# Optimization experiments

Hardware: AMD Instinct MI355X
Metric: run time of the kernel (lower is better)

## Reference

```python
import jax, jax.numpy as jnp
import numpy as np

HIDDEN = 1024
B, S = 4, 2048


def setup_inputs() -> dict:
    key = jax.random.key(0)
    ks = jax.random.split(key, 8)
    scale = 1.0 / np.sqrt(HIDDEN)
    return {
        "hidden_states": jax.random.normal(ks[0], (B, S, HIDDEN), dtype=jnp.float32),
        "attention_mask": jnp.zeros((B, S, S), dtype=jnp.float32),
        "Wq": jax.random.normal(ks[1], (HIDDEN, HIDDEN), dtype=jnp.float32) * scale,
        "bq": jnp.zeros((HIDDEN,), dtype=jnp.float32),
        "Wk": jax.random.normal(ks[2], (HIDDEN, HIDDEN), dtype=jnp.float32) * scale,
        "bk": jnp.zeros((HIDDEN,), dtype=jnp.float32),
        "Wv": jax.random.normal(ks[3], (HIDDEN, HIDDEN), dtype=jnp.float32) * scale,
        "bv": jnp.zeros((HIDDEN,), dtype=jnp.float32),
    }


def reference(hidden_states, attention_mask, Wq, bq, Wk, bk, Wv, bv):
    # Dense projections (note: no head split in the original module)
    q = jnp.einsum('bsd,de->bse', hidden_states, Wq) + bq  # [B,S,H]
    k = jnp.einsum('bsd,de->bse', hidden_states, Wk) + bk
    v = jnp.einsum('bsd,de->bse', hidden_states, Wv) + bv
    # scores scaled by sqrt(hidden_size) (not per-head dim), per the source
    inv_scale = 1.0 / jnp.sqrt(jnp.asarray(q.shape[-1], dtype=q.dtype))
    scores = jnp.einsum('bqd,bkd->bqk', q, k) * inv_scale  # [B,S,S]
    scores = scores + attention_mask
    weights = jax.nn.softmax(scores, axis=-1)
    # dropout is identity (training=False)
    out = jnp.einsum('bqk,bkd->bqd', weights, v)  # [B,S,H]
    return out
```

## Files before the change

### kernel.cpp

```cpp
#include <hip/hip_runtime.h>
#include <stdint.h>

typedef __attribute__((ext_vector_type(8))) short short8;
typedef __attribute__((ext_vector_type(8))) unsigned short u16x8;
typedef __attribute__((ext_vector_type(4))) float f32x4;

__device__ __forceinline__ uint16_t f2bf(float x) {
  uint32_t u = __float_as_uint(x);
  uint32_t r = (u + 0x7FFFu + ((u >> 16) & 1u)) >> 16;
  return (uint16_t)r;
}
__device__ __forceinline__ float bf2f(uint16_t x) {
  return __uint_as_float(((uint32_t)x) << 16);
}

__device__ __forceinline__ void gl_lds16(const uint16_t* g, void* l) {
  __builtin_amdgcn_global_load_lds(
      (const __attribute__((address_space(1))) void*)g,
      (__attribute__((address_space(3))) void*)l, 16, 0, 0);
}


__global__ __launch_bounds__(256) void cvt_f32_to_bf16(const float* __restrict__ in,
                                                       uint16_t* __restrict__ out) {
  long i = ((long)blockIdx.x * 256 + threadIdx.x) * 8;
  f32x4 v0 = *(const f32x4*)(in + i);
  f32x4 v1 = *(const f32x4*)(in + i + 4);
  u16x8 o;
  o[0] = f2bf(v0[0]); o[1] = f2bf(v0[1]); o[2] = f2bf(v0[2]); o[3] = f2bf(v0[3]);
  o[4] = f2bf(v1[0]); o[5] = f2bf(v1[1]); o[6] = f2bf(v1[2]); o[7] = f2bf(v1[3]);
  *(u16x8*)(out + i) = o;
}

__global__ __launch_bounds__(64) void cvt_w_transpose(const float* __restrict__ W0,
                                                      const float* __restrict__ W1,
                                                      const float* __restrict__ W2,
                                                      uint16_t* __restrict__ WT) {
  const int z = blockIdx.z;
  const float* W = (z == 0) ? W0 : ((z == 1) ? W1 : W2);
  uint16_t* out = WT + (long)z * 1024 * 1024;
  const int n = blockIdx.x * 64 + threadIdx.x;
  const int k0 = blockIdx.y * 128;
  for (int kk = 0; kk < 128; kk += 8) {
    u16x8 o;
#pragma unroll
    for (int j = 0; j < 8; j++) o[j] = f2bf(W[(long)(k0 + kk + j) * 1024 + n]);
    *(u16x8*)(out + (long)n * 1024 + k0 + kk) = o;
  }
}

__global__ __launch_bounds__(256) void transpose_v(const uint16_t* __restrict__ V,
                                                   uint16_t* __restrict__ Vt) {
  __shared__ uint16_t tile[64][66];
  const int b = blockIdx.z;
  const int s0 = blockIdx.x * 64, d0 = blockIdx.y * 64;
  const int t = threadIdx.x;
  const int r = t >> 3, c = (t & 7) * 8;
  const uint16_t* Vb = V + (long)b * 2048 * 1024;
#pragma unroll
  for (int j = 0; j < 2; j++) {
    u16x8 v = *(const u16x8*)(Vb + (long)(s0 + r + 32 * j) * 1024 + d0 + c);
#pragma unroll
    for (int i = 0; i < 8; i++) tile[r + 32 * j][c + i] = v[i];
  }
  __syncthreads();
  uint16_t* Vtb = Vt + (long)b * 1024 * 2048;
#pragma unroll
  for (int j = 0; j < 2; j++) {
    const int d = r + 32 * j;
    u16x8 o;
#pragma unroll
    for (int i = 0; i < 8; i++) o[i] = tile[c + i][d];
    *(u16x8*)(Vtb + (long)(d0 + d) * 2048 + s0 + c) = o;
  }
}

template <int MODE>
__global__ __launch_bounds__(512, 2) void gemm3(
    const uint16_t* __restrict__ Abase, long sAz,
    const uint16_t* __restrict__ Bbase, long sBz,
    int K, int N,
    char* __restrict__ Cbase, long sCz,
    const float* __restrict__ e0, const float* __restrict__ e1,
    const float* __restrict__ e2,
    const float* __restrict__ lsum) {
  constexpr int ABYTES = 256 * 32 * 2;
  constexpr int BBYTES = 128 * 32 * 2;
  constexpr int BUFB = ABYTES + BBYTES;
  __shared__ __align__(16) char lds[2 * BUFB];
  const int t = threadIdx.x;
  const int lane = t & 63;
  const int w = t >> 6;
  const int bm = blockIdx.x, bn = blockIdx.y, bz = blockIdx.z;
  const uint16_t* A = (const uint16_t*)((const char*)Abase + (long)bz * sAz);
  const uint16_t* Bm = (const uint16_t*)((const char*)Bbase + (long)bz * sBz);

  const int sr = t >> 2;
  const int sc = (t & 3) * 8;
  const uint16_t* ga0 = A + (long)(bm * 256 + sr) * K + sc;
  const uint16_t* ga1 = A + (long)(bm * 256 + 128 + sr) * K + sc;
  const uint16_t* gb0 = Bm + (long)(bn * 128 + sr) * K + sc;

  f32x4 acc[4][4];
#pragma unroll
  for (int i = 0; i < 4; i++)
#pragma unroll
    for (int j = 0; j < 4; j++) acc[i][j] = (f32x4){0.f, 0.f, 0.f, 0.f};

  const int wm = w >> 1, wn = w & 1;
  const int fr = lane & 15, kg = lane >> 4;
  const int aoff = (wm * 64 + fr) * 32 + kg * 8;
  const int boff = (wn * 64 + fr) * 32 + kg * 8;

#define STG(off, ko) { gl_lds16(ga0 + (ko), lds + (off) + w * 1024); \
                       gl_lds16(ga1 + (ko), lds + (off) + 8192 + w * 1024); \
                       gl_lds16(gb0 + (ko), lds + (off) + ABYTES + w * 1024); }

  STG(0, 0);

  int cur = 0;
  for (int k0 = 0; k0 < K; k0 += 32) {
    __syncthreads();
    if (k0 + 32 < K) {
      STG((cur ^ 1) * BUFB, k0 + 32);
    }
    const uint16_t* Ab = (const uint16_t*)(lds + cur * BUFB);
    const uint16_t* Bb = (const uint16_t*)(lds + cur * BUFB + ABYTES);
    short8 a[4], b[4];
#pragma unroll
    for (int i = 0; i < 4; i++) a[i] = *(const short8*)(Ab + aoff + i * 16 * 32);
#pragma unroll
    for (int j = 0; j < 4; j++) b[j] = *(const short8*)(Bb + boff + j * 16 * 32);
#pragma unroll
    for (int i = 0; i < 4; i++)
#pragma unroll
      for (int j = 0; j < 4; j++)
        acc[i][j] = __builtin_amdgcn_mfma_f32_16x16x32_bf16(a[i], b[j], acc[i][j], 0, 0, 0);
    cur ^= 1;
  }
#undef STG

  const int row0 = bm * 256 + wm * 64 + (kg << 2);
  if (MODE == 0) {
    const int zz = bn >> 3;
    const float* bias = (zz == 0) ? e0 : ((zz == 1) ? e1 : e2);
    uint16_t* C = (uint16_t*)(Cbase + (long)zz * sCz);
    const int cb = (bn & 7) * 128 + wn * 64 + fr;
#pragma unroll
    for (int i = 0; i < 4; i++) {
#pragma unroll
      for (int j = 0; j < 4; j++) {
        const float bv_ = bias[cb + j * 16];
#pragma unroll
        for (int r = 0; r < 4; r++) {
          C[(long)(row0 + i * 16 + r) * 1024 + cb + j * 16] = f2bf(acc[i][j][r] + bv_);
        }
      }
    }
  } else {
    const int col0 = bn * 128 + wn * 64 + fr;
    float* C = (float*)(Cbase + (long)bz * sCz);
    const float* ls = lsum + (long)bz * 2048;
#pragma unroll
    for (int i = 0; i < 4; i++) {
      const int rr = row0 + i * 16;
      const float ri0 = 1.0f / ls[rr], ri1 = 1.0f / ls[rr + 1];
      const float ri2 = 1.0f / ls[rr + 2], ri3 = 1.0f / ls[rr + 3];
#pragma unroll
      for (int j = 0; j < 4; j++) {
        float* dst = C + (long)rr * N + col0 + j * 16;
        dst[0] = acc[i][j][0] * ri0;
        dst[(long)N] = acc[i][j][1] * ri1;
        dst[(long)2 * N] = acc[i][j][2] * ri2;
        dst[(long)3 * N] = acc[i][j][3] * ri3;
      }
    }
  }
}

__global__ __launch_bounds__(512, 2) void gemm_sc(
    const uint16_t* __restrict__ Abase, long sAz,
    const uint16_t* __restrict__ Bbase, long sBz,
    int K, int N,
    char* __restrict__ Cbase, long sCz,
    const float* __restrict__ maskb, long sMz, float scale,
    float* __restrict__ lsum) {
  constexpr int ABYTES = 32768;
  constexpr int BUFB = 65536;
  __shared__ __align__(16) char lds[2 * BUFB];
  const int t = threadIdx.x;
  const int lane = t & 63;
  const int w = t >> 6;
  const int bm = blockIdx.x, bn = blockIdx.y, bz = blockIdx.z;
  const uint16_t* A = (const uint16_t*)((const char*)Abase + (long)bz * sAz);
  const uint16_t* B = (const uint16_t*)((const char*)Bbase + (long)bz * sBz);

  const int srow = t >> 3;
  const int scol = ((((t & 7) * 16) ^ ((srow & 7) << 4)) >> 1);
  const uint16_t* gA[4];
  const uint16_t* gB[4];
#pragma unroll
  for (int s = 0; s < 4; s++) {
    gA[s] = A + (long)(bm * 256 + s * 64 + srow) * K + scol;
    gB[s] = B + (long)(bn * 256 + s * 64 + srow) * K + scol;
  }

  const int wm = w >> 2, wn = w & 3;
  const int fr = lane & 15, kg = lane >> 4;
  const int X = (fr & 7) << 4;
  const int aRow = (wm * 128 + fr) * 128 + kg * 16;
  const int bRow = (wn * 64 + fr) * 128 + kg * 16;

  f32x4 acc[8][4];
#pragma unroll
  for (int i = 0; i < 8; i++)
#pragma unroll
    for (int j = 0; j < 4; j++) acc[i][j] = (f32x4){0.f, 0.f, 0.f, 0.f};

  short8 aR[4][2], bR[4][2];
  const int NT = K >> 6;

#define ARD(off, i, ks) (*(const short8*)(lds + (off) + ((aRow + (i) * 2048 + (ks) * 64) ^ X)))
#define BRD(off, j, ks) (*(const short8*)(lds + ABYTES + (off) + ((bRow + (j) * 2048 + (ks) * 64) ^ X)))
#define STG_A01(off, ko) { gl_lds16(gA[0] + (ko), lds + (off) + w * 1024); \
                           gl_lds16(gA[1] + (ko), lds + (off) + 8192 + w * 1024); }
#define STG_A23(off, ko) { gl_lds16(gA[2] + (ko), lds + (off) + 16384 + w * 1024); \
                           gl_lds16(gA[3] + (ko), lds + (off) + 24576 + w * 1024); }
#define STG_B01(off, ko) { gl_lds16(gB[0] + (ko), lds + ABYTES + (off) + w * 1024); \
                           gl_lds16(gB[1] + (ko), lds + ABYTES + (off) + 8192 + w * 1024); }
#define STG_B23(off, ko) { gl_lds16(gB[2] + (ko), lds + ABYTES + (off) + 16384 + w * 1024); \
                           gl_lds16(gB[3] + (ko), lds + ABYTES + (off) + 24576 + w * 1024); }
#define LGKM0 { asm volatile("s_waitcnt lgkmcnt(0)" ::: "memory"); __builtin_amdgcn_sched_barrier(0); }
#define MFMA16(I0, J0)                                                            \
  __builtin_amdgcn_s_setprio(1);                                                  \
  _Pragma("unroll") for (int i = 0; i < 4; i++)                                   \
  _Pragma("unroll") for (int j = 0; j < 2; j++)                                   \
  _Pragma("unroll") for (int ks = 0; ks < 2; ks++)                                \
    acc[(I0) + i][(J0) + j] = __builtin_amdgcn_mfma_f32_16x16x32_bf16(            \
        aR[i][ks], bR[(J0) + j][ks], acc[(I0) + i][(J0) + j], 0, 0, 0);           \
  __builtin_amdgcn_s_setprio(0);

  STG_A01(0, 0); STG_A23(0, 0); STG_B01(0, 0); STG_B23(0, 0);

  int curo = 0;
  for (int tt = 0; tt < NT - 1; ++tt) {
    const int nxto = curo ^ BUFB;
    const int ko = (tt + 1) << 6;
    STG_A01(nxto, ko);
    asm volatile("s_waitcnt vmcnt(2)" ::: "memory");
    __builtin_amdgcn_s_barrier();
    __builtin_amdgcn_sched_barrier(0);
#pragma unroll
    for (int i = 0; i < 4; i++) { aR[i][0] = ARD(curo, i, 0); aR[i][1] = ARD(curo, i, 1); }
#pragma unroll
    for (int j = 0; j < 4; j++) { bR[j][0] = BRD(curo, j, 0); bR[j][1] = BRD(curo, j, 1); }
    LGKM0;
    MFMA16(0, 0);
    __builtin_amdgcn_s_barrier();
    STG_A23(nxto, ko);
    __builtin_amdgcn_s_barrier();
    MFMA16(0, 2);
    __builtin_amdgcn_s_barrier();
    STG_B01(nxto, ko);
#pragma unroll
    for (int i = 0; i < 4; i++) { aR[i][0] = ARD(curo, 4 + i, 0); aR[i][1] = ARD(curo, 4 + i, 1); }
    __builtin_amdgcn_s_barrier();
    LGKM0;
    MFMA16(4, 2);
    __builtin_amdgcn_s_barrier();
    STG_B23(nxto, ko);
    __builtin_amdgcn_s_barrier();
    MFMA16(4, 0);
    __builtin_amdgcn_s_barrier();
    curo = nxto;
  }
  asm volatile("s_waitcnt vmcnt(0)" ::: "memory");
  __builtin_amdgcn_s_barrier();
  __builtin_amdgcn_sched_barrier(0);
#pragma unroll
  for (int i = 0; i < 4; i++) { aR[i][0] = ARD(curo, i, 0); aR[i][1] = ARD(curo, i, 1); }
#pragma unroll
  for (int j = 0; j < 4; j++) { bR[j][0] = BRD(curo, j, 0); bR[j][1] = BRD(curo, j, 1); }
  LGKM0;
  MFMA16(0, 0);
  MFMA16(0, 2);
#pragma unroll
  for (int i = 0; i < 4; i++) { aR[i][0] = ARD(curo, 4 + i, 0); aR[i][1] = ARD(curo, 4 + i, 1); }
  LGKM0;
  MFMA16(4, 2);
  MFMA16(4, 0);

  __syncthreads();
  constexpr int RS = 260;
  float* eL = (float*)lds;
  const int wboff = wm * (16 * RS) + (kg * 4) * RS + wn * 64 + fr;
  const int lr = t >> 4, slab = lr >> 4, row16 = lr & 15, cj = t & 15;
  const float* rb = eL + slab * (16 * RS) + row16 * RS + cj * 16;
  const int grow_base = bm * 256 + slab * 128 + row16;
  const int colg = bn * 256 + cj * 16;
  uint16_t* Cw = (uint16_t*)(Cbase + (long)bz * sCz);
  const float* mk = (const float*)((const char*)maskb + (long)bz * sMz);

#pragma unroll
  for (int i = 0; i < 8; i++) {
#pragma unroll
    for (int j = 0; j < 4; j++)
#pragma unroll
      for (int r = 0; r < 4; r++)
        eL[wboff + r * RS + j * 16] = acc[i][j][r];
    __syncthreads();
    f32x4 v0 = *(const f32x4*)(rb);
    f32x4 v1 = *(const f32x4*)(rb + 4);
    f32x4 v2 = *(const f32x4*)(rb + 8);
    f32x4 v3 = *(const f32x4*)(rb + 12);
    const int grow = grow_base + i * 16;
    const float* mrow = mk + (long)grow * N + colg;
    f32x4 m0 = *(const f32x4*)(mrow);
    f32x4 m1 = *(const f32x4*)(mrow + 4);
    f32x4 m2 = *(const f32x4*)(mrow + 8);
    f32x4 m3 = *(const f32x4*)(mrow + 12);
    float e[16];
#pragma unroll
    for (int q = 0; q < 4; q++) {
      e[q] = __expf(v0[q] * scale + m0[q]);
      e[4 + q] = __expf(v1[q] * scale + m1[q]);
      e[8 + q] = __expf(v2[q] * scale + m2[q]);
      e[12 + q] = __expf(v3[q] * scale + m3[q]);
    }
    float ps = 0.f;
#pragma unroll
    for (int q = 0; q < 16; q++) ps += e[q];
    ps += __shfl_xor(ps, 1);
    ps += __shfl_xor(ps, 2);
    ps += __shfl_xor(ps, 4);
    ps += __shfl_xor(ps, 8);
    if ((lane & 15) == 0) atomicAdd(lsum + (long)bz * 2048 + grow, ps);
    u16x8 o0, o1;
#pragma unroll
    for (int q = 0; q < 8; q++) { o0[q] = f2bf(e[q]); o1[q] = f2bf(e[8 + q]); }
    uint16_t* dst = Cw + (long)grow * N + colg;
    *(u16x8*)dst = o0;
    *(u16x8*)(dst + 8) = o1;
    __syncthreads();
  }
#undef ARD
#undef BRD
#undef STG_A01
#undef STG_A23
#undef STG_B01
#undef STG_B23
#undef LGKM0
#undef MFMA16
}

extern "C" void kernel_launch(void* const* d_in, const int* in_sizes, int n_in,
                              void* d_out, int out_size, void* d_ws, size_t ws_size,
                              hipStream_t stream) {
  const float* hs = (const float*)d_in[0];
  const float* mask = (const float*)d_in[1];
  const float* Wq = (const float*)d_in[2];
  const float* bq = (const float*)d_in[3];
  const float* Wk = (const float*)d_in[4];
  const float* bk = (const float*)d_in[5];
  const float* Wv = (const float*)d_in[6];
  const float* bv = (const float*)d_in[7];
  float* out = (float*)d_out;

  char* ws = (char*)d_ws;
  uint16_t* hsb = (uint16_t*)ws;
  uint16_t* WT = (uint16_t*)(ws + (16L << 20));
  uint16_t* QKV = (uint16_t*)(ws + (22L << 20));
  uint16_t* Vt = (uint16_t*)(ws + (70L << 20));
  uint16_t* E = (uint16_t*)(ws + (86L << 20));
  float* lsum = (float*)(ws + (118L << 20));

  cvt_f32_to_bf16<<<4096, 256, 0, stream>>>(hs, hsb);
  cvt_w_transpose<<<dim3(16, 8, 3), 64, 0, stream>>>(Wq, Wk, Wv, WT);
  hipMemsetAsync((void*)lsum, 0, 4L * 2048 * sizeof(float), stream);
  gemm3<0><<<dim3(32, 24, 1), 512, 0, stream>>>(
      hsb, 0L, WT, 0L, 1024, 3072, (char*)QKV, 16L << 20,
      bq, bk, bv, nullptr);
  transpose_v<<<dim3(32, 16, 4), 256, 0, stream>>>(QKV + 2L * 8192 * 1024, Vt);
  gemm_sc<<<dim3(8, 8, 4), 512, 0, stream>>>(
      QKV, 4L << 20, QKV + 8192L * 1024, 4L << 20, 1024, 2048, (char*)E, 8L << 20,
      mask, 16L << 20, 0.03125f, lsum);
  gemm3<2><<<dim3(8, 8, 4), 512, 0, stream>>>(
      E, 8L << 20, Vt, 4L << 20, 2048, 1024, (char*)out, 8L << 20,
      nullptr, nullptr, nullptr, lsum);
}
```

Before: 196.4 us.

## Remap GEMM block indices for XCD locality and shrink PV tile to 128x128

Result: no change. 197.9 us (+0.7%).

```diff
diff --git a/kernel.cpp b/kernel.cpp
--- a/kernel.cpp
+++ b/kernel.cpp
@@ -75,15 +75,12 @@
   }
 }
 
-template <int MODE>
-__global__ __launch_bounds__(512, 2) void gemm3(
-    const uint16_t* __restrict__ Abase, long sAz,
-    const uint16_t* __restrict__ Bbase, long sBz,
-    int K, int N,
+__global__ __launch_bounds__(512, 2) void gemm3_proj(
+    const uint16_t* __restrict__ A, const uint16_t* __restrict__ Bm,
     char* __restrict__ Cbase, long sCz,
     const float* __restrict__ e0, const float* __restrict__ e1,
-    const float* __restrict__ e2,
-    const float* __restrict__ lsum) {
+    const float* __restrict__ e2) {
+  constexpr int K = 1024;
   constexpr int ABYTES = 256 * 32 * 2;
   constexpr int BBYTES = 128 * 32 * 2;
   constexpr int BUFB = ABYTES + BBYTES;
@@ -91,9 +88,10 @@
   const int t = threadIdx.x;
   const int lane = t & 63;
   const int w = t >> 6;
-  const int bm = blockIdx.x, bn = blockIdx.y, bz = blockIdx.z;
-  const uint16_t* A = (const uint16_t*)((const char*)Abase + (long)bz * sAz);
-  const uint16_t* Bm = (const uint16_t*)((const char*)Bbase + (long)bz * sBz);
+  const int hw = blockIdx.x;
+  const int x = hw & 7, c = hw >> 3;
+  const int bm = ((x >> 1) << 3) + (c & 7);
+  const int bn = (x & 1) * 12 + (c >> 3);
 
   const int sr = t >> 2;
   const int sc = (t & 3) * 8;
@@ -115,17 +113,100 @@
 #define STG(off, ko) { gl_lds16(ga0 + (ko), lds + (off) + w * 1024); \
                        gl_lds16(ga1 + (ko), lds + (off) + 8192 + w * 1024); \
                        gl_lds16(gb0 + (ko), lds + (off) + ABYTES + w * 1024); }
-
   STG(0, 0);
+  int cur = 0;
+  for (int k0 = 0; k0 < K; k0 += 32) {
+    __syncthreads();
+    if (k0 + 32 < K) STG((cur ^ 1) * BUFB, k0 + 32);
+    const uint16_t* Ab = (const uint16_t*)(lds + cur * BUFB);
+    const uint16_t* Bb = (const uint16_t*)(lds + cur * BUFB + ABYTES);
+    short8 a[4], b[4];
+#pragma unroll
+    for (int i = 0; i < 4; i++) a[i] = *(const short8*)(Ab + aoff + i * 16 * 32);
+#pragma unroll
+    for (int j = 0; j < 4; j++) b[j] = *(const short8*)(Bb + boff + j * 16 * 32);
+#pragma unroll
+    for (int i = 0; i < 4; i++)
+#pragma unroll
+      for (int j = 0; j < 4; j++)
+        acc[i][j] = __builtin_amdgcn_mfma_f32_16x16x32_bf16(a[i], b[j], acc[i][j], 0, 0, 0);
+    cur ^= 1;
+  }
+#undef STG
+
+  const int row0 = bm * 256 + wm * 64 + (kg << 2);
+  const int zz = bn >> 3;
+  const float* bias = (zz == 0) ? e0 : ((zz == 1) ? e1 : e2);
+  uint16_t* C = (uint16_t*)(Cbase + (long)zz * sCz);
+  const int cb = (bn & 7) * 128 + wn * 64 + fr;
+#pragma unroll
+  for (int i = 0; i < 4; i++) {
+#pragma unroll
+    for (int j = 0; j < 4; j++) {
+      const float bv_ = bias[cb + j * 16];
+#pragma unroll
+      for (int r = 0; r < 4; r++) {
+        C[(long)(row0 + i * 16 + r) * 1024 + cb + j * 16] = f2bf(acc[i][j][r] + bv_);
+      }
+    }
+  }
+}
+
+__global__ __launch_bounds__(256) void gemm_pv(
+    const uint16_t* __restrict__ Abase, long sAz,
+    const uint16_t* __restrict__ Bbase, long sBz,
+    int K, int N,
+    float* __restrict__ Cbase, long sCzf,
+    const float* __restrict__ lsum) {
+  __shared__ uint16_t Al[2][128 * 32];
+  __shared__ uint16_t Bl[2][128 * 32];
+  const int t = threadIdx.x;
+  const int lane = t & 63;
+  const int w = t >> 6;
+  const int hw = blockIdx.x;
+  const int x = hw & 7, c = hw >> 3;
+  const int bz = x & 3;
+  const int bm = ((x >> 2) << 3) + (c & 7);
+  const int bn = c >> 3;
+
+  const uint16_t* A = (const uint16_t*)((const char*)Abase + (long)bz * sAz);
+  const uint16_t* Bm = (const uint16_t*)((const char*)Bbase + (long)bz * sBz);
+
+  const int sr = t >> 2;
+  const int sc = (t & 3) * 8;
+  const uint16_t* ga0 = A + (long)(bm * 128 + sr) * K + sc;
+  const uint16_t* ga1 = A + (long)(bm * 128 + 64 + sr) * K + sc;
+  const uint16_t* gb0 = Bm + (long)(bn * 128 + sr) * K + sc;
+  const uint16_t* gb1 = Bm + (long)(bn * 128 + 64 + sr) * K + sc;
+
+  f32x4 acc[4][4];
+#pragma unroll
+  for (int i = 0; i < 4; i++)
+#pragma unroll
+    for (int j = 0; j < 4; j++) acc[i][j] = (f32x4){0.f, 0.f, 0.f, 0.f};
+
+  const int wm = w >> 1, wn = w & 1;
+  const int fr = lane & 15, kg = lane >> 4;
+  const int aoff = (wm * 64 + fr) * 32 + kg * 8;
+  const int boff = (wn * 64 + fr) * 32 + kg * 8;
+
+  gl_lds16(ga0, Al[0] + w * 512);
+  gl_lds16(ga1, Al[0] + 2048 + w * 512);
+  gl_lds16(gb0, Bl[0] + w * 512);
+  gl_lds16(gb1, Bl[0] + 2048 + w * 512);
 
   int cur = 0;
   for (int k0 = 0; k0 < K; k0 += 32) {
     __syncthreads();
     if (k0 + 32 < K) {
-      STG((cur ^ 1) * BUFB, k0 + 32);
+      const int nb = cur ^ 1, kn = k0 + 32;
+      gl_lds16(ga0 + kn, Al[nb] + w * 512);
+      gl_lds16(ga1 + kn, Al[nb] + 2048 + w * 512);
+      gl_lds16(gb0 + kn, Bl[nb] + w * 512);
+      gl_lds16(gb1 + kn, Bl[nb] + 2048 + w * 512);
     }
-    const uint16_t* Ab = (const uint16_t*)(lds + cur * BUFB);
-    const uint16_t* Bb = (const uint16_t*)(lds + cur * BUFB + ABYTES);
+    const uint16_t* Ab = Al[cur];
+    const uint16_t* Bb = Bl[cur];
     short8 a[4], b[4];
 #pragma unroll
     for (int i = 0; i < 4; i++) a[i] = *(const short8*)(Ab + aoff + i * 16 * 32);
@@ -138,42 +219,23 @@
         acc[i][j] = __builtin_amdgcn_mfma_f32_16x16x32_bf16(a[i], b[j], acc[i][j], 0, 0, 0);
     cur ^= 1;
   }
-#undef STG
-
-  const int row0 = bm * 256 + wm * 64 + (kg << 2);
-  if (MODE == 0) {
-    const int zz = bn >> 3;
-    const float* bias = (zz == 0) ? e0 : ((zz == 1) ? e1 : e2);
-    uint16_t* C = (uint16_t*)(Cbase + (long)zz * sCz);
-    const int cb = (bn & 7) * 128 + wn * 64 + fr;
-#pragma unroll
-    for (int i = 0; i < 4; i++) {
-#pragma unroll
-      for (int j = 0; j < 4; j++) {
-        const float bv_ = bias[cb + j * 16];
-#pragma unroll
-        for (int r = 0; r < 4; r++) {
-          C[(long)(row0 + i * 16 + r) * 1024 + cb + j * 16] = f2bf(acc[i][j][r] + bv_);
-        }
-      }
-    }
-  } else {
-    const int col0 = bn * 128 + wn * 64 + fr;
-    float* C = (float*)(Cbase + (long)bz * sCz);
-    const float* ls = lsum + (long)bz * 2048;
-#pragma unroll
-    for (int i = 0; i < 4; i++) {
-      const int rr = row0 + i * 16;
-      const float ri0 = 1.0f / ls[rr], ri1 = 1.0f / ls[rr + 1];
-      const float ri2 = 1.0f / ls[rr + 2], ri3 = 1.0f / ls[rr + 3];
-#pragma unroll
-      for (int j = 0; j < 4; j++) {
-        float* dst = C + (long)rr * N + col0 + j * 16;
-        dst[0] = acc[i][j][0] * ri0;
-        dst[(long)N] = acc[i][j][1] * ri1;
-        dst[(long)2 * N] = acc[i][j][2] * ri2;
-        dst[(long)3 * N] = acc[i][j][3] * ri3;
-      }
+
+  const int row0 = bm * 128 + wm * 64 + (kg << 2);
+  const int col0 = bn * 128 + wn * 64 + fr;
+  float* C = Cbase + (long)bz * sCzf;
+  const float* ls = lsum + (long)bz * 2048;
+#pragma unroll
+  for (int i = 0; i < 4; i++) {
+    const int rr = row0 + i * 16;
+    const float ri0 = 1.0f / ls[rr], ri1 = 1.0f / ls[rr + 1];
+    const float ri2 = 1.0f / ls[rr + 2], ri3 = 1.0f / ls[rr + 3];
+#pragma unroll
+    for (int j = 0; j < 4; j++) {
+      float* dst = C + (long)rr * N + col0 + j * 16;
+      dst[0] = acc[i][j][0] * ri0;
+      dst[(long)N] = acc[i][j][1] * ri1;
+      dst[(long)2 * N] = acc[i][j][2] * ri2;
+      dst[(long)3 * N] = acc[i][j][3] * ri3;
     }
   }
 }
@@ -191,7 +253,11 @@
   const int t = threadIdx.x;
   const int lane = t & 63;
   const int w = t >> 6;
-  const int bm = blockIdx.x, bn = blockIdx.y, bz = blockIdx.z;
+  const int hw = blockIdx.x;
+  const int x = hw & 7, c = hw >> 3;
+  const int bz = x & 3;
+  const int bm = c & 7;
+  const int bn = ((x >> 2) << 2) + (c >> 3);
   const uint16_t* A = (const uint16_t*)((const char*)Abase + (long)bz * sAz);
   const uint16_t* B = (const uint16_t*)((const char*)Bbase + (long)bz * sBz);
 
@@ -377,14 +443,12 @@
   cvt_f32_to_bf16<<<4096, 256, 0, stream>>>(hs, hsb);
   cvt_w_transpose<<<dim3(16, 8, 3), 64, 0, stream>>>(Wq, Wk, Wv, WT);
   hipMemsetAsync((void*)lsum, 0, 4L * 2048 * sizeof(float), stream);
-  gemm3<0><<<dim3(32, 24, 1), 512, 0, stream>>>(
-      hsb, 0L, WT, 0L, 1024, 3072, (char*)QKV, 16L << 20,
-      bq, bk, bv, nullptr);
+  gemm3_proj<<<768, 512, 0, stream>>>(
+      hsb, WT, (char*)QKV, 16L << 20, bq, bk, bv);
   transpose_v<<<dim3(32, 16, 4), 256, 0, stream>>>(QKV + 2L * 8192 * 1024, Vt);
-  gemm_sc<<<dim3(8, 8, 4), 512, 0, stream>>>(
+  gemm_sc<<<256, 512, 0, stream>>>(
       QKV, 4L << 20, QKV + 8192L * 1024, 4L << 20, 1024, 2048, (char*)E, 8L << 20,
       mask, 16L << 20, 0.03125f, lsum);
-  gemm3<2><<<dim3(8, 8, 4), 512, 0, stream>>>(
-      E, 8L << 20, Vt, 4L << 20, 2048, 1024, (char*)out, 8L << 20,
-      nullptr, nullptr, nullptr, lsum);
-}
+  gemm_pv<<<512, 256, 0, stream>>>(
+      E, 8L << 20, Vt, 4L << 20, 2048, 1024, out, 2048L * 1024, lsum);
+}
```
